# Kernel optimization log

Hardware: AMD Instinct MI355X
Metric: run time of the kernel (lower is better)

The kernel has to match this reference:

```python
import jax, jax.numpy as jnp
import numpy as np

H = 1024

def setup_inputs() -> dict:
    key = jax.random.key(0)
    k1, k2, k3, k4, k5 = jax.random.split(key, 5)
    B, T = 32, 2048
    s = 1.0 / np.sqrt(H)
    return {
        "decoder_state": jax.random.normal(k1, (B, H), dtype=jnp.float32),
        "encoder_states": jax.random.normal(k2, (B, T, H), dtype=jnp.float32),
        "Wa_w": jax.random.uniform(k3, (H, H), jnp.float32, -s, s),
        "Wa_b": jnp.zeros((H,), jnp.float32),
        "Ua_w": jax.random.uniform(k4, (H, H), jnp.float32, -s, s),
        "Ua_b": jnp.zeros((H,), jnp.float32),
        "v_w": jax.random.uniform(k5, (H,), jnp.float32, -s, s),
        "v_b": jnp.zeros((), jnp.float32),
    }

def reference(decoder_state, encoder_states, Wa_w, Wa_b, Ua_w, Ua_b, v_w, v_b):
    # decoder_state: [B,H], encoder_states: [B,T,H]
    dec_proj = decoder_state @ Ua_w.T + Ua_b            # [B,H]
    enc_proj = jnp.einsum('bth,oh->bto', encoder_states, Wa_w) + Wa_b  # [B,T,H]
    e = jnp.tanh(dec_proj[:, None, :] + enc_proj)        # [B,T,H]
    scores = jnp.einsum('bth,h->bt', e, v_w) + v_b       # [B,T]
    attn_weights = jax.nn.softmax(scores, axis=1)        # [B,T]
    context = jnp.einsum('bt,bth->bh', attn_weights, encoder_states)  # [B,H]
    return (context, attn_weights)
```

## Files before the change

kernel.cpp:

```cpp
#include <hip/hip_runtime.h>
#include <hip/hip_bf16.h>

#define HH 1024
#define BB 32
#define TT 2048

typedef __attribute__((ext_vector_type(8))) short bf16x8;
typedef __attribute__((ext_vector_type(4))) float f32x4;

static __device__ __forceinline__ unsigned short f2bf(float f) {
    unsigned int u = __float_as_uint(f);
    unsigned int r = u + 0x7fffu + ((u >> 16) & 1u);
    return (unsigned short)(r >> 16);
}
static __device__ __forceinline__ float bf2f(unsigned short u) {
    return __uint_as_float(((unsigned int)u) << 16);
}
static __device__ __forceinline__ float fast_tanh(float x) {
    float e = __expf(2.0f * x);
    return 1.0f - 2.0f / (e + 1.0f);
}

#define GLOAD_LDS16(gp, lp) \
    __builtin_amdgcn_global_load_lds( \
        (const __attribute__((address_space(1))) void*)(gp), \
        (__attribute__((address_space(3))) void*)(lp), 16, 0, 0)

__global__ void k_convW(const float* __restrict__ W, unsigned short* __restrict__ Wb) {
    int i = blockIdx.x * 256 + threadIdx.x;
    float4 v = ((const float4*)W)[i];
    ushort4 o;
    o.x = f2bf(v.x); o.y = f2bf(v.y); o.z = f2bf(v.z); o.w = f2bf(v.w);
    ((ushort4*)Wb)[i] = o;
}

__global__ void k_convEnc(const float* __restrict__ E, unsigned short* __restrict__ Eb) {
    long i = ((long)blockIdx.x * 256 + threadIdx.x) * 8;
    float4 a = *(const float4*)(E + i);
    float4 b = *(const float4*)(E + i + 4);
    ushort4 o0, o1;
    o0.x = f2bf(a.x); o0.y = f2bf(a.y); o0.z = f2bf(a.z); o0.w = f2bf(a.w);
    o1.x = f2bf(b.x); o1.y = f2bf(b.y); o1.z = f2bf(b.z); o1.w = f2bf(b.w);
    *(ushort4*)(Eb + i) = o0;
    *(ushort4*)(Eb + i + 4) = o1;
}

__global__ void k_decproj(const float* __restrict__ dec, const float* __restrict__ Ua,
                          const float* __restrict__ Uab, const float* __restrict__ Wab,
                          float* __restrict__ dp) {
    int gtid = blockIdx.x * 256 + threadIdx.x;
    int b = gtid >> 10, o = gtid & 1023;
    const float4* d4 = (const float4*)(dec + (long)b * HH);
    const float4* u4 = (const float4*)(Ua + (long)o * HH);
    float acc = 0.f;
    for (int k = 0; k < HH / 4; ++k) {
        float4 a = d4[k], w = u4[k];
        acc += a.x * w.x + a.y * w.y + a.z * w.z + a.w * w.w;
    }
    dp[gtid] = acc + Uab[o] + Wab[o];
}

__global__ __launch_bounds__(512) void k_score_bf(
        const unsigned short* __restrict__ encb, const unsigned short* __restrict__ Wb,
        const float* __restrict__ dp, const float* __restrict__ vw,
        float* __restrict__ scores) {
    __shared__ __align__(16) unsigned short As[2][256 * 64];
    __shared__ __align__(16) unsigned short Bs[2][256 * 64];
    int bid = blockIdx.x;
    int xcd = bid & 7;
    int ord = bid >> 3;
    int nt = ord & 3;
    int mt = (ord >> 2) * 8 + xcd;
    long m0 = (long)mt * 256;
    int o0b = nt * 256;
    int tid = threadIdx.x;
    int lane = tid & 63, wid = tid >> 6;
    int wm = wid >> 2, wn = wid & 3;
    int r = lane & 15, g = lane >> 4;

    f32x4 acc[8][4];
    #pragma unroll
    for (int i = 0; i < 8; ++i)
        #pragma unroll
        for (int j = 0; j < 4; ++j) acc[i][j] = (f32x4){0.f, 0.f, 0.f, 0.f};

    int srow = tid >> 3;
    int swu = (tid & 7) ^ (srow & 7);
    const unsigned short* aSrc = encb + (m0 + srow) * HH + swu * 8;
    const unsigned short* bSrc = Wb + (long)(o0b + srow) * HH + swu * 8;
    int ldso = wid * 512;
    int rx = r & 7;
    int u0 = (g ^ rx) * 8;
    int u1 = ((4 + g) ^ rx) * 8;

    #pragma unroll
    for (int p = 0; p < 4; ++p) {
        GLOAD_LDS16(aSrc + p * 64 * HH, &As[0][ldso + p * 4096]);
        GLOAD_LDS16(bSrc + p * 64 * HH, &Bs[0][ldso + p * 4096]);
    }
    __syncthreads();

    #pragma unroll 1
    for (int t = 0; t < 16; ++t) {
        int bi = t & 1, pi = bi ^ 1;
        int kc2 = (t + 1) * 64;
        bool pre = (t < 15);

        bf16x8 bfr[4][2];
        #pragma unroll
        for (int ni = 0; ni < 4; ++ni) {
            int rowb = (wn * 64 + ni * 16 + r) * 64;
            bfr[ni][0] = *(const bf16x8*)(&Bs[bi][rowb + u0]);
            bfr[ni][1] = *(const bf16x8*)(&Bs[bi][rowb + u1]);
        }
        bf16x8 aq[2][2][2];
        #pragma unroll
        for (int q = 0; q < 2; ++q) {
            int rowa = (wm * 128 + q * 16 + r) * 64;
            aq[0][q][0] = *(const bf16x8*)(&As[bi][rowa + u0]);
            aq[0][q][1] = *(const bf16x8*)(&As[bi][rowa + u1]);
        }

        #pragma unroll
        for (int p = 0; p < 4; ++p) {
            if (pre && p < 2) {
                GLOAD_LDS16(aSrc + kc2 + (2 * p) * 64 * HH,
                            &As[pi][ldso + (2 * p) * 4096]);
                GLOAD_LDS16(aSrc + kc2 + (2 * p + 1) * 64 * HH,
                            &As[pi][ldso + (2 * p + 1) * 4096]);
                GLOAD_LDS16(bSrc + kc2 + (2 * p) * 64 * HH,
                            &Bs[pi][ldso + (2 * p) * 4096]);
                GLOAD_LDS16(bSrc + kc2 + (2 * p + 1) * 64 * HH,
                            &Bs[pi][ldso + (2 * p + 1) * 4096]);
            }
            if (p < 3) {
                #pragma unroll
                for (int q = 0; q < 2; ++q) {
                    int rowa = (wm * 128 + (2 * (p + 1) + q) * 16 + r) * 64;
                    aq[(p + 1) & 1][q][0] = *(const bf16x8*)(&As[bi][rowa + u0]);
                    aq[(p + 1) & 1][q][1] = *(const bf16x8*)(&As[bi][rowa + u1]);
                }
            }
            __builtin_amdgcn_s_setprio(1);
            #pragma unroll
            for (int q = 0; q < 2; ++q) {
                int mi = 2 * p + q;
                #pragma unroll
                for (int ni = 0; ni < 4; ++ni) {
                    acc[mi][ni] = __builtin_amdgcn_mfma_f32_16x16x32_bf16(
                        aq[p & 1][q][0], bfr[ni][0], acc[mi][ni], 0, 0, 0);
                    acc[mi][ni] = __builtin_amdgcn_mfma_f32_16x16x32_bf16(
                        aq[p & 1][q][1], bfr[ni][1], acc[mi][ni], 0, 0, 0);
                }
            }
            __builtin_amdgcn_s_setprio(0);
        }
        __syncthreads();
    }

    int bb = (int)(m0 >> 11);
    float vv[4], dpv[4];
    #pragma unroll
    for (int ni = 0; ni < 4; ++ni) {
        int o = o0b + wn * 64 + ni * 16 + r;
        vv[ni] = vw[o];
        dpv[ni] = dp[bb * HH + o];
    }
    #pragma unroll
    for (int mi = 0; mi < 8; ++mi) {
        float vp[4] = {0.f, 0.f, 0.f, 0.f};
        #pragma unroll
        for (int ni = 0; ni < 4; ++ni)
            #pragma unroll
            for (int j = 0; j < 4; ++j)
                vp[j] += fast_tanh(acc[mi][ni][j] + dpv[ni]) * vv[ni];
        #pragma unroll
        for (int j = 0; j < 4; ++j) {
            float s = vp[j];
            s += __shfl_xor(s, 1); s += __shfl_xor(s, 2);
            s += __shfl_xor(s, 4); s += __shfl_xor(s, 8);
            if (r == 0) {
                int row = wm * 128 + mi * 16 + g * 4 + j;
                atomicAdd(&scores[m0 + row], s);
            }
        }
    }
}

#define LDSP 40
__global__ __launch_bounds__(256) void k_score(const float* __restrict__ enc,
        const unsigned short* __restrict__ Wb, const float* __restrict__ dp,
        const float* __restrict__ vw, float* __restrict__ scores) {
    __shared__ __align__(16) unsigned short As[128][LDSP];
    __shared__ __align__(16) unsigned short Bs[128][LDSP];
    int bid = blockIdx.x;
    int nt = bid & 7;
    int mt = bid >> 3;
    long m0 = (long)mt * 128;
    int o0 = nt * 128;
    int tid = threadIdx.x;
    int lane = tid & 63, wid = tid >> 6;
    int wm = wid >> 1, wn = wid & 1;
    int r = lane & 15, g = lane >> 4;

    f32x4 acc[4][4];
    #pragma unroll
    for (int i = 0; i < 4; ++i)
        #pragma unroll
        for (int j = 0; j < 4; ++j) acc[i][j] = (f32x4){0.f, 0.f, 0.f, 0.f};

    for (int kc = 0; kc < HH; kc += 32) {
        #pragma unroll
        for (int i = 0; i < 4; ++i) {
            int idx = tid + i * 256;
            int row = idx >> 3, kq = idx & 7;
            float4 a = *(const float4*)(enc + (m0 + row) * HH + kc + kq * 4);
            ushort4 p;
            p.x = f2bf(a.x); p.y = f2bf(a.y); p.z = f2bf(a.z); p.w = f2bf(a.w);
            *(ushort4*)(&As[row][kq * 4]) = p;
        }
        #pragma unroll
        for (int i = 0; i < 2; ++i) {
            int idx = tid + i * 256;
            int row = idx >> 2, kq = idx & 3;
            *(int4*)(&Bs[row][kq * 8]) =
                *(const int4*)(Wb + (long)(o0 + row) * HH + kc + kq * 8);
        }
        __syncthreads();
        bf16x8 af[4], bfr[4];
        #pragma unroll
        for (int mi = 0; mi < 4; ++mi)
            af[mi] = *(const bf16x8*)(&As[wm * 64 + mi * 16 + r][g * 8]);
        #pragma unroll
        for (int ni = 0; ni < 4; ++ni)
            bfr[ni] = *(const bf16x8*)(&Bs[wn * 64 + ni * 16 + r][g * 8]);
        #pragma unroll
        for (int mi = 0; mi < 4; ++mi)
            #pragma unroll
            for (int ni = 0; ni < 4; ++ni)
                acc[mi][ni] = __builtin_amdgcn_mfma_f32_16x16x32_bf16(
                    af[mi], bfr[ni], acc[mi][ni], 0, 0, 0);
        __syncthreads();
    }

    int bb = (int)(m0 >> 11);
    #pragma unroll
    for (int mi = 0; mi < 4; ++mi) {
        float vp[4] = {0.f, 0.f, 0.f, 0.f};
        #pragma unroll
        for (int ni = 0; ni < 4; ++ni) {
            int o = o0 + wn * 64 + ni * 16 + r;
            float vvs = vw[o];
            float dpvs = dp[bb * HH + o];
            #pragma unroll
            for (int j = 0; j < 4; ++j)
                vp[j] += fast_tanh(acc[mi][ni][j] + dpvs) * vvs;
        }
        #pragma unroll
        for (int j = 0; j < 4; ++j) {
            float s = vp[j];
            s += __shfl_xor(s, 1); s += __shfl_xor(s, 2);
            s += __shfl_xor(s, 4); s += __shfl_xor(s, 8);
            if (r == 0) {
                int row = wm * 64 + mi * 16 + g * 4 + j;
                atomicAdd(&scores[m0 + row], s);
            }
        }
    }
}

__global__ void k_softmax(float* __restrict__ w) {
    int b = blockIdx.x;
    float* row = w + (long)b * TT;
    int tid = threadIdx.x;
    float loc[8];
    float m = -1e30f;
    #pragma unroll
    for (int i = 0; i < 8; ++i) { loc[i] = row[tid + i * 256]; m = fmaxf(m, loc[i]); }
    #pragma unroll
    for (int off = 1; off < 64; off <<= 1) m = fmaxf(m, __shfl_xor(m, off));
    __shared__ float red[4];
    if ((tid & 63) == 0) red[tid >> 6] = m;
    __syncthreads();
    m = fmaxf(fmaxf(red[0], red[1]), fmaxf(red[2], red[3]));
    float s = 0.f;
    #pragma unroll
    for (int i = 0; i < 8; ++i) { loc[i] = __expf(loc[i] - m); s += loc[i]; }
    #pragma unroll
    for (int off = 1; off < 64; off <<= 1) s += __shfl_xor(s, off);
    __shared__ float red2[4];
    if ((tid & 63) == 0) red2[tid >> 6] = s;
    __syncthreads();
    s = red2[0] + red2[1] + red2[2] + red2[3];
    float inv = 1.0f / s;
    #pragma unroll
    for (int i = 0; i < 8; ++i) row[tid + i * 256] = loc[i] * inv;
}

__global__ void k_context_bf(const unsigned short* __restrict__ encb,
                             const float* __restrict__ w, float* __restrict__ ctx) {
    int bid = blockIdx.x;
    int b = bid >> 4;
    int ts = bid & 15;
    int h = threadIdx.x * 4;
    const float* wr = w + (long)b * TT + ts * 128;
    long base = ((long)b * TT + (long)ts * 128) * HH + h;
    float a0 = 0.f, a1 = 0.f, a2 = 0.f, a3 = 0.f;
    #pragma unroll 4
    for (int t = 0; t < 128; ++t) {
        ushort4 e = *(const ushort4*)(encb + base + (long)t * HH);
        float ww = wr[t];
        a0 += ww * bf2f(e.x);
        a1 += ww * bf2f(e.y);
        a2 += ww * bf2f(e.z);
        a3 += ww * bf2f(e.w);
    }
    atomicAdd(&ctx[b * HH + h], a0);
    atomicAdd(&ctx[b * HH + h + 1], a1);
    atomicAdd(&ctx[b * HH + h + 2], a2);
    atomicAdd(&ctx[b * HH + h + 3], a3);
}

__global__ void k_context(const float* __restrict__ enc, const float* __restrict__ w,
                          float* __restrict__ ctx) {
    int bid = blockIdx.x;
    int b = bid >> 6;
    int hc = (bid >> 4) & 3;
    int ts = bid & 15;
    int h = hc * 256 + threadIdx.x;
    const float* wr = w + (long)b * TT + ts * 128;
    long base = ((long)b * TT + (long)ts * 128) * HH + h;
    float acc = 0.f;
    for (int t = 0; t < 128; ++t)
        acc += wr[t] * enc[base + (long)t * HH];
    atomicAdd(&ctx[b * HH + h], acc);
}

extern "C" void kernel_launch(void* const* d_in, const int* in_sizes, int n_in,
                              void* d_out, int out_size, void* d_ws, size_t ws_size,
                              hipStream_t stream) {
    const float* dec  = (const float*)d_in[0];
    const float* enc  = (const float*)d_in[1];
    const float* Wa_w = (const float*)d_in[2];
    const float* Wa_b = (const float*)d_in[3];
    const float* Ua_w = (const float*)d_in[4];
    const float* Ua_b = (const float*)d_in[5];
    const float* v_w  = (const float*)d_in[6];

    float* out  = (float*)d_out;
    float* ctx  = out;
    float* attn = out + BB * HH;

    float* dpw = (float*)d_ws;
    unsigned short* Wb = (unsigned short*)((char*)d_ws + 131072);
    unsigned short* encb = (unsigned short*)((char*)d_ws + 131072 + 2097152);
    const size_t NEED = 131072ull + 2097152ull + (size_t)BB * TT * HH * 2;

    hipMemsetAsync(d_out, 0, (size_t)out_size * sizeof(float), stream);
    k_convW<<<1024, 256, 0, stream>>>(Wa_w, Wb);
    k_decproj<<<128, 256, 0, stream>>>(dec, Ua_w, Ua_b, Wa_b, dpw);

    if (ws_size >= NEED) {
        k_convEnc<<<32768, 256, 0, stream>>>(enc, encb);
        k_score_bf<<<1024, 512, 0, stream>>>(encb, Wb, dpw, v_w, attn);
        k_softmax<<<BB, 256, 0, stream>>>(attn);
        k_context_bf<<<512, 256, 0, stream>>>(encb, attn, ctx);
    } else {
        k_score<<<4096, 256, 0, stream>>>(enc, Wb, dpw, v_w, attn);
        k_softmax<<<BB, 256, 0, stream>>>(attn);
        k_context<<<2048, 256, 0, stream>>>(enc, attn, ctx);
    }
}
```

Baseline: 292.7 us.

## Restructure GEMM main loop into barrier-synchronised phases with split A/B prefetch

Replaces the register double-buffered A-fragment prefetch with per-phase LDS reads, each phase bracketed by workgroup barriers and explicit lgkmcnt waits. The next-tile global-to-LDS loads are split so A is issued in phase 0 and B in phase 1. The end-of-tile __syncthreads becomes an explicit vmcnt wait plus s_barrier. The aim is to keep waves in lockstep so MFMA bursts interleave better across waves. In exchange it adds eight barriers per K tile and drops the overlap of LDS reads with the previous MFMA block.

After: 299.6 us. 1.02x slower.

```diff
diff --git a/kernel.cpp b/kernel.cpp
--- a/kernel.cpp
+++ b/kernel.cpp
@@ -102,45 +102,43 @@
 
     #pragma unroll 1
     for (int t = 0; t < 16; ++t) {
-        int bi = t & 1, pi = bi ^ 1;
-        int kc2 = (t + 1) * 64;
-        bool pre = (t < 15);
-
+        const int bi = t & 1, pi = bi ^ 1;
+        const int kc2 = (t + 1) * 64;
+        const bool pre = (t < 15);
         bf16x8 bfr[4][2];
-        #pragma unroll
-        for (int ni = 0; ni < 4; ++ni) {
-            int rowb = (wn * 64 + ni * 16 + r) * 64;
-            bfr[ni][0] = *(const bf16x8*)(&Bs[bi][rowb + u0]);
-            bfr[ni][1] = *(const bf16x8*)(&Bs[bi][rowb + u1]);
-        }
-        bf16x8 aq[2][2][2];
-        #pragma unroll
-        for (int q = 0; q < 2; ++q) {
-            int rowa = (wm * 128 + q * 16 + r) * 64;
-            aq[0][q][0] = *(const bf16x8*)(&As[bi][rowa + u0]);
-            aq[0][q][1] = *(const bf16x8*)(&As[bi][rowa + u1]);
-        }
 
         #pragma unroll
         for (int p = 0; p < 4; ++p) {
-            if (pre && p < 2) {
-                GLOAD_LDS16(aSrc + kc2 + (2 * p) * 64 * HH,
-                            &As[pi][ldso + (2 * p) * 4096]);
-                GLOAD_LDS16(aSrc + kc2 + (2 * p + 1) * 64 * HH,
-                            &As[pi][ldso + (2 * p + 1) * 4096]);
-                GLOAD_LDS16(bSrc + kc2 + (2 * p) * 64 * HH,
-                            &Bs[pi][ldso + (2 * p) * 4096]);
-                GLOAD_LDS16(bSrc + kc2 + (2 * p + 1) * 64 * HH,
-                            &Bs[pi][ldso + (2 * p + 1) * 4096]);
-            }
-            if (p < 3) {
+            bf16x8 aqr[2][2];
+            #pragma unroll
+            for (int q = 0; q < 2; ++q) {
+                int rowa = (wm * 128 + (2 * p + q) * 16 + r) * 64;
+                aqr[q][0] = *(const bf16x8*)(&As[bi][rowa + u0]);
+                aqr[q][1] = *(const bf16x8*)(&As[bi][rowa + u1]);
+            }
+            if (p == 0) {
                 #pragma unroll
-                for (int q = 0; q < 2; ++q) {
-                    int rowa = (wm * 128 + (2 * (p + 1) + q) * 16 + r) * 64;
-                    aq[(p + 1) & 1][q][0] = *(const bf16x8*)(&As[bi][rowa + u0]);
-                    aq[(p + 1) & 1][q][1] = *(const bf16x8*)(&As[bi][rowa + u1]);
+                for (int ni = 0; ni < 4; ++ni) {
+                    int rowb = (wn * 64 + ni * 16 + r) * 64;
+                    bfr[ni][0] = *(const bf16x8*)(&Bs[bi][rowb + u0]);
+                    bfr[ni][1] = *(const bf16x8*)(&Bs[bi][rowb + u1]);
                 }
             }
+            if (pre && p == 0) {
+                #pragma unroll
+                for (int q = 0; q < 4; ++q)
+                    GLOAD_LDS16(aSrc + kc2 + q * 64 * HH,
+                                &As[pi][ldso + q * 4096]);
+            }
+            if (pre && p == 1) {
+                #pragma unroll
+                for (int q = 0; q < 4; ++q)
+                    GLOAD_LDS16(bSrc + kc2 + q * 64 * HH,
+                                &Bs[pi][ldso + q * 4096]);
+            }
+            __builtin_amdgcn_s_barrier();
+            asm volatile("s_waitcnt lgkmcnt(0)" ::: "memory");
+            __builtin_amdgcn_sched_barrier(0);
             __builtin_amdgcn_s_setprio(1);
             #pragma unroll
             for (int q = 0; q < 2; ++q) {
@@ -148,14 +146,16 @@
                 #pragma unroll
                 for (int ni = 0; ni < 4; ++ni) {
                     acc[mi][ni] = __builtin_amdgcn_mfma_f32_16x16x32_bf16(
-                        aq[p & 1][q][0], bfr[ni][0], acc[mi][ni], 0, 0, 0);
+                        aqr[q][0], bfr[ni][0], acc[mi][ni], 0, 0, 0);
                     acc[mi][ni] = __builtin_amdgcn_mfma_f32_16x16x32_bf16(
-                        aq[p & 1][q][1], bfr[ni][1], acc[mi][ni], 0, 0, 0);
+                        aqr[q][1], bfr[ni][1], acc[mi][ni], 0, 0, 0);
                 }
             }
             __builtin_amdgcn_s_setprio(0);
-        }
-        __syncthreads();
+            if (p == 3 && pre)
+                asm volatile("s_waitcnt vmcnt(0)" ::: "memory");
+            __builtin_amdgcn_s_barrier();
+        }
     }
 
     int bb = (int)(m0 >> 11);
```

## Fuse fp32-to-bf16 encoder conversion into score GEMM and drop bf16 copy

Applied to the files above, without the earlier changes.

Removes the separate pass that converted the whole encoder tensor to bf16 in workspace. The score GEMM now loads fp32 encoder tiles into registers, converts them with packed bf16 conversion instructions and stores them to LDS after the MFMA work of each k-step. The context kernel reads fp32 encoder data directly. This trades the extra write-and-reread of a bf16 copy for register-staged A loads, which may reduce the overlap that the earlier direct global-to-LDS path gave.

New measurement: 265.1 us. -9.4%, faster.

```diff
diff --git a/kernel.cpp b/kernel.cpp
--- a/kernel.cpp
+++ b/kernel.cpp
@@ -13,8 +13,10 @@
     unsigned int r = u + 0x7fffu + ((u >> 16) & 1u);
     return (unsigned short)(r >> 16);
 }
-static __device__ __forceinline__ float bf2f(unsigned short u) {
-    return __uint_as_float(((unsigned int)u) << 16);
+static __device__ __forceinline__ unsigned int cvt_pk_bf16(float lo, float hi) {
+    unsigned int d;
+    asm volatile("v_cvt_pk_bf16_f32 %0, %1, %2" : "=v"(d) : "v"(lo), "v"(hi));
+    return d;
 }
 static __device__ __forceinline__ float fast_tanh(float x) {
     float e = __expf(2.0f * x);
@@ -32,17 +34,6 @@
     ushort4 o;
     o.x = f2bf(v.x); o.y = f2bf(v.y); o.z = f2bf(v.z); o.w = f2bf(v.w);
     ((ushort4*)Wb)[i] = o;
-}
-
-__global__ void k_convEnc(const float* __restrict__ E, unsigned short* __restrict__ Eb) {
-    long i = ((long)blockIdx.x * 256 + threadIdx.x) * 8;
-    float4 a = *(const float4*)(E + i);
-    float4 b = *(const float4*)(E + i + 4);
-    ushort4 o0, o1;
-    o0.x = f2bf(a.x); o0.y = f2bf(a.y); o0.z = f2bf(a.z); o0.w = f2bf(a.w);
-    o1.x = f2bf(b.x); o1.y = f2bf(b.y); o1.z = f2bf(b.z); o1.w = f2bf(b.w);
-    *(ushort4*)(Eb + i) = o0;
-    *(ushort4*)(Eb + i + 4) = o1;
 }
 
 __global__ void k_decproj(const float* __restrict__ dec, const float* __restrict__ Ua,
@@ -61,7 +52,7 @@
 }
 
 __global__ __launch_bounds__(512) void k_score_bf(
-        const unsigned short* __restrict__ encb, const unsigned short* __restrict__ Wb,
+        const float* __restrict__ enc, const unsigned short* __restrict__ Wb,
         const float* __restrict__ dp, const float* __restrict__ vw,
         float* __restrict__ scores) {
     __shared__ __align__(16) unsigned short As[2][256 * 64];
@@ -85,18 +76,35 @@
         for (int j = 0; j < 4; ++j) acc[i][j] = (f32x4){0.f, 0.f, 0.f, 0.f};
 
     int srow = tid >> 3;
-    int swu = (tid & 7) ^ (srow & 7);
-    const unsigned short* aSrc = encb + (m0 + srow) * HH + swu * 8;
+    int acol = (tid & 7) * 8;
+    int awu = (tid & 7) ^ (srow & 7);
+    int swu = awu;
+    const float* aSrcF = enc + (m0 + srow) * HH + acol;
     const unsigned short* bSrc = Wb + (long)(o0b + srow) * HH + swu * 8;
     int ldso = wid * 512;
     int rx = r & 7;
     int u0 = (g ^ rx) * 8;
     int u1 = ((4 + g) ^ rx) * 8;
 
-    #pragma unroll
-    for (int p = 0; p < 4; ++p) {
-        GLOAD_LDS16(aSrc + p * 64 * HH, &As[0][ldso + p * 4096]);
-        GLOAD_LDS16(bSrc + p * 64 * HH, &Bs[0][ldso + p * 4096]);
+    int aw0 = srow * 64 + awu * 8;
+
+    {
+        float4 ar[8];
+        #pragma unroll
+        for (int q = 0; q < 4; ++q) {
+            ar[2 * q]     = *(const float4*)(aSrcF + (long)64 * q * HH);
+            ar[2 * q + 1] = *(const float4*)(aSrcF + (long)64 * q * HH + 4);
+            GLOAD_LDS16(bSrc + (long)q * 64 * HH, &Bs[0][ldso + q * 4096]);
+        }
+        #pragma unroll
+        for (int q = 0; q < 4; ++q) {
+            uint4 w;
+            w.x = cvt_pk_bf16(ar[2 * q].x, ar[2 * q].y);
+            w.y = cvt_pk_bf16(ar[2 * q].z, ar[2 * q].w);
+            w.z = cvt_pk_bf16(ar[2 * q + 1].x, ar[2 * q + 1].y);
+            w.w = cvt_pk_bf16(ar[2 * q + 1].z, ar[2 * q + 1].w);
+            *(uint4*)(&As[0][aw0 + q * 4096]) = w;
+        }
     }
     __syncthreads();
 
@@ -105,6 +113,7 @@
         int bi = t & 1, pi = bi ^ 1;
         int kc2 = (t + 1) * 64;
         bool pre = (t < 15);
+        float4 ar[8];
 
         bf16x8 bfr[4][2];
         #pragma unroll
@@ -123,15 +132,18 @@
 
         #pragma unroll
         for (int p = 0; p < 4; ++p) {
-            if (pre && p < 2) {
-                GLOAD_LDS16(aSrc + kc2 + (2 * p) * 64 * HH,
-                            &As[pi][ldso + (2 * p) * 4096]);
-                GLOAD_LDS16(aSrc + kc2 + (2 * p + 1) * 64 * HH,
-                            &As[pi][ldso + (2 * p + 1) * 4096]);
-                GLOAD_LDS16(bSrc + kc2 + (2 * p) * 64 * HH,
-                            &Bs[pi][ldso + (2 * p) * 4096]);
-                GLOAD_LDS16(bSrc + kc2 + (2 * p + 1) * 64 * HH,
-                            &Bs[pi][ldso + (2 * p + 1) * 4096]);
+            if (pre && p == 0) {
+                #pragma unroll
+                for (int q = 0; q < 4; ++q) {
+                    ar[2 * q]     = *(const float4*)(aSrcF + (long)64 * q * HH + kc2);
+                    ar[2 * q + 1] = *(const float4*)(aSrcF + (long)64 * q * HH + kc2 + 4);
+                }
+                GLOAD_LDS16(bSrc + kc2 + (long)0 * 64 * HH, &Bs[pi][ldso + 0 * 4096]);
+                GLOAD_LDS16(bSrc + kc2 + (long)1 * 64 * HH, &Bs[pi][ldso + 1 * 4096]);
+            }
+            if (pre && p == 1) {
+                GLOAD_LDS16(bSrc + kc2 + (long)2 * 64 * HH, &Bs[pi][ldso + 2 * 4096]);
+                GLOAD_LDS16(bSrc + kc2 + (long)3 * 64 * HH, &Bs[pi][ldso + 3 * 4096]);
             }
             if (p < 3) {
                 #pragma unroll
@@ -155,6 +167,17 @@
             }
             __builtin_amdgcn_s_setprio(0);
         }
+        if (pre) {
+            #pragma unroll
+            for (int q = 0; q < 4; ++q) {
+                uint4 w;
+                w.x = cvt_pk_bf16(ar[2 * q].x, ar[2 * q].y);
+                w.y = cvt_pk_bf16(ar[2 * q].z, ar[2 * q].w);
+                w.z = cvt_pk_bf16(ar[2 * q + 1].x, ar[2 * q + 1].y);
+                w.w = cvt_pk_bf16(ar[2 * q + 1].z, ar[2 * q + 1].w);
+                *(uint4*)(&As[pi][aw0 + q * 4096]) = w;
+            }
+        }
         __syncthreads();
     }
 
@@ -187,88 +210,6 @@
     }
 }
 
-#define LDSP 40
-__global__ __launch_bounds__(256) void k_score(const float* __restrict__ enc,
-        const unsigned short* __restrict__ Wb, const float* __restrict__ dp,
-        const float* __restrict__ vw, float* __restrict__ scores) {
-    __shared__ __align__(16) unsigned short As[128][LDSP];
-    __shared__ __align__(16) unsigned short Bs[128][LDSP];
-    int bid = blockIdx.x;
-    int nt = bid & 7;
-    int mt = bid >> 3;
-    long m0 = (long)mt * 128;
-    int o0 = nt * 128;
-    int tid = threadIdx.x;
-    int lane = tid & 63, wid = tid >> 6;
-    int wm = wid >> 1, wn = wid & 1;
-    int r = lane & 15, g = lane >> 4;
-
-    f32x4 acc[4][4];
-    #pragma unroll
-    for (int i = 0; i < 4; ++i)
-        #pragma unroll
-        for (int j = 0; j < 4; ++j) acc[i][j] = (f32x4){0.f, 0.f, 0.f, 0.f};
-
-    for (int kc = 0; kc < HH; kc += 32) {
-        #pragma unroll
-        for (int i = 0; i < 4; ++i) {
-            int idx = tid + i * 256;
-            int row = idx >> 3, kq = idx & 7;
-            float4 a = *(const float4*)(enc + (m0 + row) * HH + kc + kq * 4);
-            ushort4 p;
-            p.x = f2bf(a.x); p.y = f2bf(a.y); p.z = f2bf(a.z); p.w = f2bf(a.w);
-            *(ushort4*)(&As[row][kq * 4]) = p;
-        }
-        #pragma unroll
-        for (int i = 0; i < 2; ++i) {
-            int idx = tid + i * 256;
-            int row = idx >> 2, kq = idx & 3;
-            *(int4*)(&Bs[row][kq * 8]) =
-                *(const int4*)(Wb + (long)(o0 + row) * HH + kc + kq * 8);
-        }
-        __syncthreads();
-        bf16x8 af[4], bfr[4];
-        #pragma unroll
-        for (int mi = 0; mi < 4; ++mi)
-            af[mi] = *(const bf16x8*)(&As[wm * 64 + mi * 16 + r][g * 8]);
-        #pragma unroll
-        for (int ni = 0; ni < 4; ++ni)
-            bfr[ni] = *(const bf16x8*)(&Bs[wn * 64 + ni * 16 + r][g * 8]);
-        #pragma unroll
-        for (int mi = 0; mi < 4; ++mi)
-            #pragma unroll
-            for (int ni = 0; ni < 4; ++ni)
-                acc[mi][ni] = __builtin_amdgcn_mfma_f32_16x16x32_bf16(
-                    af[mi], bfr[ni], acc[mi][ni], 0, 0, 0);
-        __syncthreads();
-    }
-
-    int bb = (int)(m0 >> 11);
-    #pragma unroll
-    for (int mi = 0; mi < 4; ++mi) {
-        float vp[4] = {0.f, 0.f, 0.f, 0.f};
-        #pragma unroll
-        for (int ni = 0; ni < 4; ++ni) {
-            int o = o0 + wn * 64 + ni * 16 + r;
-            float vvs = vw[o];
-            float dpvs = dp[bb * HH + o];
-            #pragma unroll
-            for (int j = 0; j < 4; ++j)
-                vp[j] += fast_tanh(acc[mi][ni][j] + dpvs) * vvs;
-        }
-        #pragma unroll
-        for (int j = 0; j < 4; ++j) {
-            float s = vp[j];
-            s += __shfl_xor(s, 1); s += __shfl_xor(s, 2);
-            s += __shfl_xor(s, 4); s += __shfl_xor(s, 8);
-            if (r == 0) {
-                int row = wm * 64 + mi * 16 + g * 4 + j;
-                atomicAdd(&scores[m0 + row], s);
-            }
-        }
-    }
-}
-
 __global__ void k_softmax(float* __restrict__ w) {
     int b = blockIdx.x;
     float* row = w + (long)b * TT;
@@ -295,30 +236,6 @@
     float inv = 1.0f / s;
     #pragma unroll
     for (int i = 0; i < 8; ++i) row[tid + i * 256] = loc[i] * inv;
-}
-
-__global__ void k_context_bf(const unsigned short* __restrict__ encb,
-                             const float* __restrict__ w, float* __restrict__ ctx) {
-    int bid = blockIdx.x;
-    int b = bid >> 4;
-    int ts = bid & 15;
-    int h = threadIdx.x * 4;
-    const float* wr = w + (long)b * TT + ts * 128;
-    long base = ((long)b * TT + (long)ts * 128) * HH + h;
-    float a0 = 0.f, a1 = 0.f, a2 = 0.f, a3 = 0.f;
-    #pragma unroll 4
-    for (int t = 0; t < 128; ++t) {
-        ushort4 e = *(const ushort4*)(encb + base + (long)t * HH);
-        float ww = wr[t];
-        a0 += ww * bf2f(e.x);
-        a1 += ww * bf2f(e.y);
-        a2 += ww * bf2f(e.z);
-        a3 += ww * bf2f(e.w);
-    }
-    atomicAdd(&ctx[b * HH + h], a0);
-    atomicAdd(&ctx[b * HH + h + 1], a1);
-    atomicAdd(&ctx[b * HH + h + 2], a2);
-    atomicAdd(&ctx[b * HH + h + 3], a3);
 }
 
 __global__ void k_context(const float* __restrict__ enc, const float* __restrict__ w,
@@ -331,6 +248,7 @@
     const float* wr = w + (long)b * TT + ts * 128;
     long base = ((long)b * TT + (long)ts * 128) * HH + h;
     float acc = 0.f;
+    #pragma unroll 4
     for (int t = 0; t < 128; ++t)
         acc += wr[t] * enc[base + (long)t * HH];
     atomicAdd(&ctx[b * HH + h], acc);
@@ -353,21 +271,11 @@
 
     float* dpw = (float*)d_ws;
     unsigned short* Wb = (unsigned short*)((char*)d_ws + 131072);
-    unsigned short* encb = (unsigned short*)((char*)d_ws + 131072 + 2097152);
-    const size_t NEED = 131072ull + 2097152ull + (size_t)BB * TT * HH * 2;
 
     hipMemsetAsync(d_out, 0, (size_t)out_size * sizeof(float), stream);
     k_convW<<<1024, 256, 0, stream>>>(Wa_w, Wb);
     k_decproj<<<128, 256, 0, stream>>>(dec, Ua_w, Ua_b, Wa_b, dpw);
-
-    if (ws_size >= NEED) {
-        k_convEnc<<<32768, 256, 0, stream>>>(enc, encb);
-        k_score_bf<<<1024, 512, 0, stream>>>(encb, Wb, dpw, v_w, attn);
-        k_softmax<<<BB, 256, 0, stream>>>(attn);
-        k_context_bf<<<512, 256, 0, stream>>>(encb, attn, ctx);
-    } else {
-        k_score<<<4096, 256, 0, stream>>>(enc, Wb, dpw, v_w, attn);
-        k_softmax<<<BB, 256, 0, stream>>>(attn);
-        k_context<<<2048, 256, 0, stream>>>(enc, attn, ctx);
-    }
-}
+    k_score_bf<<<1024, 512, 0, stream>>>(enc, Wb, dpw, v_w, attn);
+    k_softmax<<<BB, 256, 0, stream>>>(attn);
+    k_context<<<2048, 256, 0, stream>>>(enc, attn, ctx);
+}
```
